# Performance work log

Measured on AMD Instinct MI355X. Metric: run time of the kernel, lower is better.

Reference implementation:

```python
import jax, jax.numpy as jnp
import numpy as np

B, T, H, NH, L, V, FF = 2, 1024, 1024, 16, 6, 8192, 4096
D = H // NH
EPS = 1e-5


def _ln(x, g, b):
    mu = jnp.mean(x, axis=-1, keepdims=True)
    var = jnp.mean(jnp.square(x - mu), axis=-1, keepdims=True)
    return (x - mu) * jax.lax.rsqrt(var + EPS) * g + b


def setup_inputs() -> dict:
    key = jax.random.key(0)
    ks = jax.random.split(key, 12)
    s = 1.0 / np.sqrt(H)
    return {
        "x": jax.random.randint(ks[0], (B, T), 0, V),
        "tok_emb": jax.random.normal(ks[1], (V, H), jnp.float32) * s,
        "pos_emb": jax.random.normal(ks[2], (1, T, H), jnp.float32) * s,
        "Wq": jax.random.normal(ks[3], (L, H, H), jnp.float32) * s,
        "bq": jnp.zeros((L, H), jnp.float32),
        "Wk": jax.random.normal(ks[4], (L, H, H), jnp.float32) * s,
        "bk": jnp.zeros((L, H), jnp.float32),
        "Wv": jax.random.normal(ks[5], (L, H, H), jnp.float32) * s,
        "bv": jnp.zeros((L, H), jnp.float32),
        "Wo": jax.random.normal(ks[6], (L, H, H), jnp.float32) * s,
        "bo": jnp.zeros((L, H), jnp.float32),
        "W1": jax.random.normal(ks[7], (L, H, FF), jnp.float32) * s,
        "b1": jnp.zeros((L, FF), jnp.float32),
        "W2": jax.random.normal(ks[8], (L, FF, H), jnp.float32) * (1.0 / np.sqrt(FF)),
        "b2": jnp.zeros((L, H), jnp.float32),
        "ln1_g": jnp.ones((L, H), jnp.float32),
        "ln1_b": jnp.zeros((L, H), jnp.float32),
        "ln2_g": jnp.ones((L, H), jnp.float32),
        "ln2_b": jnp.zeros((L, H), jnp.float32),
        "lnf_g": jnp.ones((H,), jnp.float32),
        "lnf_b": jnp.zeros((H,), jnp.float32),
        "headW": jax.random.normal(ks[9], (H, V), jnp.float32) * s,
        "headb": jnp.zeros((V,), jnp.float32),
    }


def _transformer(x, tok_emb, pos_emb, Wq, bq, Wk, bk, Wv, bv, Wo, bo,
                 W1, b1, W2, b2, ln1_g, ln1_b, ln2_g, ln2_b, lnf_g, lnf_b,
                 headW, headb):
    Tcur = x.shape[1]
    h = tok_emb[x] + pos_emb[:, :Tcur, :]            # [B,T,H]
    mask = jnp.tril(jnp.ones((Tcur, Tcur), bool))    # causal [T,T]
    scale = 1.0 / np.sqrt(D)

    def block(h, p):
        (wq, q_b, wk, k_b, wv, v_b, wo, o_b,
         w1, b1_, w2, b2_, g1, be1, g2, be2) = p
        q = (h @ wq + q_b).reshape(B, Tcur, NH, D)
        k = (h @ wk + k_b).reshape(B, Tcur, NH, D)
        v = (h @ wv + v_b).reshape(B, Tcur, NH, D)
        att = jnp.einsum('bqnd,bknd->bnqk', q, k) * scale
        att = jnp.where(mask, att, -jnp.inf)
        w = jax.nn.softmax(att, axis=-1)
        o = jnp.einsum('bnqk,bknd->bqnd', w, v).reshape(B, Tcur, H)
        h = _ln(h + (o @ wo + o_b), g1, be1)          # post-LN after attention
        m = jax.nn.gelu(h @ w1 + b1_, approximate=False) @ w2 + b2_
        h = _ln(h + m, g2, be2)                       # post-LN after MLP
        return h, None

    params = (Wq, bq, Wk, bk, Wv, bv, Wo, bo, W1, b1, W2, b2,
              ln1_g, ln1_b, ln2_g, ln2_b)
    h, _ = jax.lax.scan(block, h, params)
    h = _ln(h, lnf_g, lnf_b)
    return h @ headW + headb                          # [B,T,V]


def reference(x, tok_emb, pos_emb, Wq, bq, Wk, bk, Wv, bv, Wo, bo,
              W1, b1, W2, b2, ln1_g, ln1_b, ln2_g, ln2_b, lnf_g, lnf_b,
              headW, headb):
    return _transformer(x, tok_emb, pos_emb, Wq, bq, Wk, bk, Wv, bv, Wo, bo,
                        W1, b1, W2, b2, ln1_g, ln1_b, ln2_g, ln2_b,
                        lnf_g, lnf_b, headW, headb)
```

## Files before the change

### kernel.cpp

```cpp
#include <hip/hip_runtime.h>
#include <hip/hip_bf16.h>

#define DEV __device__ __forceinline__

typedef unsigned short u16;
typedef __attribute__((ext_vector_type(8))) short bf16x8;
typedef __attribute__((ext_vector_type(4))) float f32x4;

static constexpr int MB_ = 2;
static constexpr int T_  = 1024;
static constexpr int H_  = 1024;
static constexpr int NH_ = 16;
static constexpr int L_  = 6;
static constexpr int V_  = 8192;
static constexpr int FF_ = 4096;
static constexpr int M_  = MB_ * T_;
static constexpr int QKVN = 3 * H_;

DEV u16 f2bf(float x) {
  __hip_bfloat16 h = __float2bfloat16(x);
  return *reinterpret_cast<u16*>(&h);
}

__global__ __launch_bounds__(256) void embed_concat_kernel(
    const int* __restrict__ x, const float* __restrict__ tok,
    const float* __restrict__ pos, float* __restrict__ h, u16* __restrict__ hb,
    const float* __restrict__ bq, const float* __restrict__ bk,
    const float* __restrict__ bv, float* __restrict__ outb)
{
  int i = blockIdx.x;
  if (i < M_) {
    int t = threadIdx.x;
    int id = x[i];
    int tt = i & (T_ - 1);
    float4 a = *(const float4*)(tok + (size_t)id * H_ + t * 4);
    float4 b = *(const float4*)(pos + (size_t)tt * H_ + t * 4);
    float4 r = make_float4(a.x + b.x, a.y + b.y, a.z + b.z, a.w + b.w);
    *(float4*)(h + (size_t)i * H_ + t * 4) = r;
    ushort4 u = make_ushort4(f2bf(r.x), f2bf(r.y), f2bf(r.z), f2bf(r.w));
    *(ushort4*)(hb + (size_t)i * H_ + t * 4) = u;
  } else {
    int l = i - M_;
    for (int j = threadIdx.x; j < H_; j += 256) {
      outb[(size_t)l * QKVN + j]          = bq[(size_t)l * H_ + j];
      outb[(size_t)l * QKVN + H_ + j]     = bk[(size_t)l * H_ + j];
      outb[(size_t)l * QKVN + 2 * H_ + j] = bv[(size_t)l * H_ + j];
    }
  }
}

DEV void transpose_tile128s(float (*Ts)[65], const float* __restrict__ W,
                            u16* __restrict__ WT, int R, int C, int bx, int by)
{
  const int t = threadIdx.x;
  const int lr = t >> 4;
  const int lcq = (t & 15) * 4;
  #pragma unroll
  for (int si = 0; si < 2; ++si) {
    #pragma unroll
    for (int sj = 0; sj < 2; ++sj) {
      const int r0 = by * 128 + si * 64, c0 = bx * 128 + sj * 64;
      #pragma unroll
      for (int it = 0; it < 4; ++it) {
        int r = it * 16 + lr;
        float4 v = *(const float4*)(W + (size_t)(r0 + r) * C + c0 + lcq);
        Ts[r][lcq + 0] = v.x; Ts[r][lcq + 1] = v.y;
        Ts[r][lcq + 2] = v.z; Ts[r][lcq + 3] = v.w;
      }
      __syncthreads();
      #pragma unroll
      for (int it = 0; it < 4; ++it) {
        int n = it * 16 + lr;
        ushort4 u = make_ushort4(f2bf(Ts[lcq + 0][n]), f2bf(Ts[lcq + 1][n]),
                                 f2bf(Ts[lcq + 2][n]), f2bf(Ts[lcq + 3][n]));
        *(ushort4*)(WT + (size_t)(c0 + n) * R + r0 + lcq) = u;
      }
      __syncthreads();
    }
  }
}

DEV void transpose_layer_body(float (*Ts)[65], int t,
    const float* Wq, const float* Wk, const float* Wv, const float* Wo,
    const float* W1, const float* W2,
    u16* qkvT, u16* oT, u16* w1T, u16* w2T)
{
  if (t < 256) {
    int m = t >> 6, idx = t & 63, bx = idx & 7, by = idx >> 3;
    const float* W = (m == 0) ? Wq : (m == 1) ? Wk : (m == 2) ? Wv : Wo;
    u16* WT = (m == 3) ? oT : qkvT + (size_t)m * H_ * H_;
    transpose_tile128s(Ts, W, WT, H_, H_, bx, by);
  } else if (t < 512) {
    int idx = t - 256;
    transpose_tile128s(Ts, W1, w1T, H_, FF_, idx & 31, idx >> 5);
  } else {
    int idx = t - 512;
    transpose_tile128s(Ts, W2, w2T, FF_, H_, idx & 7, idx >> 3);
  }
}

__global__ __launch_bounds__(256) void transpose_layer_k(
    const float* __restrict__ Wq, const float* __restrict__ Wk,
    const float* __restrict__ Wv, const float* __restrict__ Wo,
    const float* __restrict__ W1, const float* __restrict__ W2,
    u16* qkvT, u16* oT, u16* w1T, u16* w2T)
{
  __shared__ float Ts[64][65];
  transpose_layer_body(Ts, blockIdx.x, Wq, Wk, Wv, Wo, W1, W2, qkvT, oT, w1T, w2T);
}


#define GLOAD_LDS16(g, l)                                              \
  __builtin_amdgcn_global_load_lds(                                    \
      (const __attribute__((address_space(1))) void*)(g),              \
      (__attribute__((address_space(3))) void*)(l), 16, 0, 0)

DEV void stage_t(const u16* __restrict__ G, int ldk, int r0g, int kofs,
                 u16* lds, int w, int lane)
{
  const int rl = ((lane >> 3) << 1) | ((lane >> 2) & 1);
  #pragma unroll
  for (int j = 0; j < 2; ++j) {
    const int row0 = w * 32 + j * 16;
    const int row = row0 + rl;
    const int c = (lane & 3) ^ (((row0 >> 1) + (lane >> 3)) & 3);
    const u16* g = G + (size_t)(r0g + row) * ldk + kofs + c * 8;
    GLOAD_LDS16(g, lds + row0 * 32);
  }
}

DEV bf16x8 frag3(const u16* lds, int rr, int ch) {
  return *(const bf16x8*)(lds + (rr >> 1) * 64 + (rr & 1) * 32 +
                          ((ch ^ ((rr >> 1) & 3)) * 8));
}

template<int N>
DEV void wait_vm_barrier() {
  asm volatile("s_waitcnt vmcnt(%0)" :: "n"(N) : "memory");
  __builtin_amdgcn_s_barrier();
}

DEV void comp3(const u16* As, const u16* Bs, f32x4 (&acc)[4][4],
               int wr, int wc, int lc, int lg)
{
  bf16x8 af[4], bv[4];
  #pragma unroll
  for (int mi = 0; mi < 4; ++mi)
    af[mi] = frag3(As, wr * 64 + mi * 16 + lc, lg);
  #pragma unroll
  for (int ni = 0; ni < 4; ++ni)
    bv[ni] = frag3(Bs, wc * 64 + ni * 16 + lc, lg);
  #pragma unroll
  for (int mi = 0; mi < 4; ++mi)
    #pragma unroll
    for (int ni = 0; ni < 4; ++ni)
      acc[mi][ni] = __builtin_amdgcn_mfma_f32_16x16x32_bf16(af[mi], bv[ni], acc[mi][ni], 0, 0, 0);
}

template<bool PARTIAL, bool DO_GELU, bool WF, bool WB>
DEV void gemm_body(u16* SMEM,
    const u16* __restrict__ A, const u16* __restrict__ BT,
    const float* __restrict__ bias, float* __restrict__ Cf,
    u16* __restrict__ Cb, float* __restrict__ P,
    int N, int K, int Ksub, int lid, int nwgx, int nwgy, int zid)
{
  const int tid = threadIdx.x;
  const int lane = tid & 63, w = tid >> 6;
  const int wr = w >> 1, wc = w & 1;
  const int lc = lane & 15, lg = lane >> 4;

  const int nwg = nwgx * nwgy;
  const int q8 = nwg >> 3, r8s = nwg & 7;
  const int xcd = lid & 7, ord = lid >> 3;
  const int sid = (xcd < r8s ? xcd * (q8 + 1) : r8s * (q8 + 1) + (xcd - r8s) * q8) + ord;
  const int m0 = (sid % nwgy) * 128, n0 = (sid / nwgy) * 128;

  const int kb = zid * Ksub;
  const int NT = Ksub >> 5;

  f32x4 acc[4][4];
  #pragma unroll
  for (int i = 0; i < 4; ++i)
    #pragma unroll
    for (int j = 0; j < 4; ++j) {
      f32x4 z = {0.f, 0.f, 0.f, 0.f};
      acc[i][j] = z;
    }

  auto STG = [&](int t, int b) {
    stage_t(A,  K, m0, kb + t * 32, SMEM + b * 4096, w, lane);
    stage_t(BT, K, n0, kb + t * 32, SMEM + 16384 + b * 4096, w, lane);
  };

  STG(0, 0);
  STG(1, 1);
  int t = 0;
  for (; t < NT - 2; ++t) {
    STG(t + 2, (t + 2) & 3);
    wait_vm_barrier<8>();
    comp3(SMEM + (t & 3) * 4096, SMEM + 16384 + (t & 3) * 4096, acc, wr, wc, lc, lg);
  }
  wait_vm_barrier<4>();
  comp3(SMEM + (t & 3) * 4096, SMEM + 16384 + (t & 3) * 4096, acc, wr, wc, lc, lg);
  ++t;
  wait_vm_barrier<0>();
  comp3(SMEM + (t & 3) * 4096, SMEM + 16384 + (t & 3) * 4096, acc, wr, wc, lc, lg);

  const size_t zofs = (size_t)zid * M_ * N;
  #pragma unroll
  for (int mi = 0; mi < 4; ++mi) {
    #pragma unroll
    for (int ni = 0; ni < 4; ++ni) {
      int gn = n0 + wc * 64 + ni * 16 + lc;
      float bvv = PARTIAL ? 0.f : bias[gn];
      #pragma unroll
      for (int r = 0; r < 4; ++r) {
        int gm = m0 + wr * 64 + mi * 16 + lg * 4 + r;
        float v = acc[mi][ni][r];
        if (PARTIAL) {
          P[zofs + (size_t)gm * N + gn] = v;
        } else {
          v += bvv;
          if (DO_GELU) v = 0.5f * v * (1.f + erff(v * 0.70710678118654752f));
          if (WF) Cf[(size_t)gm * N + gn] = v;
          if (WB) Cb[(size_t)gm * N + gn] = f2bf(v);
        }
      }
    }
  }
}

template<bool PARTIAL, bool DO_GELU, bool WF, bool WB>
__global__ __launch_bounds__(256, 2) void gemm3(
    const u16* __restrict__ A, const u16* __restrict__ BT,
    const float* __restrict__ bias, float* __restrict__ Cf,
    u16* __restrict__ Cb, float* __restrict__ P, int N, int K, int Ksub)
{
  __shared__ __align__(16) u16 SMEM[32768];
  gemm_body<PARTIAL, DO_GELU, WF, WB>(SMEM, A, BT, bias, Cf, Cb, P, N, K, Ksub,
      blockIdx.y * gridDim.x + blockIdx.x, gridDim.x, gridDim.y, blockIdx.z);
}

__global__ __launch_bounds__(256, 2) void gemmW1_fused(
    const u16* __restrict__ A, const u16* __restrict__ w1T,
    const float* __restrict__ bias, u16* __restrict__ m1,
    const float* nWq, const float* nWk, const float* nWv, const float* nWo,
    const float* nW1, const float* nW2,
    u16* nqkvT, u16* noT, u16* nw1T, u16* nw2T,
    const float* hW, u16* hT)
{
  __shared__ __align__(16) u16 SMEM[32768];
  const int id = blockIdx.x;
  if (id < 512) {
    gemm_body<false, true, false, true>(SMEM, A, w1T, bias, nullptr, m1, nullptr,
                                        FF_, H_, H_, id, 32, 16, 0);
  } else if (nWq) {
    float (*Ts)[65] = (float(*)[65])SMEM;
    transpose_layer_body(Ts, id - 512, nWq, nWk, nWv, nWo, nW1, nW2,
                         nqkvT, noT, nw1T, nw2T);
  } else {
    float (*Ts)[65] = (float(*)[65])SMEM;
    int idx = id - 512;
    transpose_tile128s(Ts, hW, hT, H_, V_, idx & 63, idx >> 6);
  }
}

__global__ __launch_bounds__(256) void ln_kernel(
    const float* __restrict__ X,
    const float* __restrict__ g, const float* __restrict__ be,
    u16* __restrict__ Hb)
{
  __shared__ float red[8];
  int row = blockIdx.x, t = threadIdx.x;
  int lane = t & 63, w = t >> 6;
  float4 v = *(const float4*)(X + (size_t)row * H_ + t * 4);
  float s = v.x + v.y + v.z + v.w;
  float q = v.x * v.x + v.y * v.y + v.z * v.z + v.w * v.w;
  #pragma unroll
  for (int o = 1; o < 64; o <<= 1) { s += __shfl_xor(s, o); q += __shfl_xor(q, o); }
  if (lane == 0) { red[w] = s; red[4 + w] = q; }
  __syncthreads();
  float S = red[0] + red[1] + red[2] + red[3];
  float Q = red[4] + red[5] + red[6] + red[7];
  float mu  = S * (1.f / H_);
  float var = Q * (1.f / H_) - mu * mu;
  float inv = rsqrtf(var + 1e-5f);
  float4 gv = *(const float4*)(g  + t * 4);
  float4 bv = *(const float4*)(be + t * 4);
  ushort4 u = make_ushort4(f2bf((v.x - mu) * inv * gv.x + bv.x),
                           f2bf((v.y - mu) * inv * gv.y + bv.y),
                           f2bf((v.z - mu) * inv * gv.z + bv.z),
                           f2bf((v.w - mu) * inv * gv.w + bv.w));
  *(ushort4*)(Hb + (size_t)row * H_ + t * 4) = u;
}

__global__ __launch_bounds__(256) void ln2_kernel(
    const float* __restrict__ P, int S,
    const float* __restrict__ bias,
    const float* __restrict__ g, const float* __restrict__ be,
    float* __restrict__ h, u16* __restrict__ hb)
{
  __shared__ float red[8];
  int row = blockIdx.x, t = threadIdx.x;
  int lane = t & 63, w = t >> 6;
  float4 v = *(const float4*)(h + (size_t)row * H_ + t * 4);
  float4 bb = *(const float4*)(bias + t * 4);
  v.x += bb.x; v.y += bb.y; v.z += bb.z; v.w += bb.w;
  for (int s0 = 0; s0 < S; ++s0) {
    float4 p = *(const float4*)(P + (size_t)s0 * M_ * H_ + (size_t)row * H_ + t * 4);
    v.x += p.x; v.y += p.y; v.z += p.z; v.w += p.w;
  }
  float s = v.x + v.y + v.z + v.w;
  float q = v.x * v.x + v.y * v.y + v.z * v.z + v.w * v.w;
  #pragma unroll
  for (int o = 1; o < 64; o <<= 1) { s += __shfl_xor(s, o); q += __shfl_xor(q, o); }
  if (lane == 0) { red[w] = s; red[4 + w] = q; }
  __syncthreads();
  float S1 = red[0] + red[1] + red[2] + red[3];
  float Q1 = red[4] + red[5] + red[6] + red[7];
  float mu  = S1 * (1.f / H_);
  float var = Q1 * (1.f / H_) - mu * mu;
  float inv = rsqrtf(var + 1e-5f);
  float4 gv = *(const float4*)(g  + t * 4);
  float4 bv = *(const float4*)(be + t * 4);
  float o0 = (v.x - mu) * inv * gv.x + bv.x;
  float o1 = (v.y - mu) * inv * gv.y + bv.y;
  float o2 = (v.z - mu) * inv * gv.z + bv.z;
  float o3 = (v.w - mu) * inv * gv.w + bv.w;
  *(float4*)(h + (size_t)row * H_ + t * 4) = make_float4(o0, o1, o2, o3);
  ushort4 u = make_ushort4(f2bf(o0), f2bf(o1), f2bf(o2), f2bf(o3));
  *(ushort4*)(hb + (size_t)row * H_ + t * 4) = u;
}

__global__ __launch_bounds__(256) void attn_kernel(
    const u16* __restrict__ qkv, u16* __restrict__ Og)
{
  __shared__ __align__(16) u16 Ks[2][64][72];
  __shared__ __align__(16) u16 Vs[2][64][72];
  __shared__ __align__(16) u16 QPs[4][16][72];

  const int qb = gridDim.x - 1 - blockIdx.x;
  const int bh = blockIdx.y;
  const int b = bh >> 4, hh = bh & 15;
  const int q0 = qb * 64;
  const size_t base  = ((size_t)b * T_) * QKVN + (size_t)hh * 64;
  const size_t baseO = ((size_t)b * T_) * H_ + (size_t)hh * 64;

  const int tid = threadIdx.x;
  const int lane = tid & 63, w = tid >> 6;
  const int lc = lane & 15, lg = lane >> 4;

  const int r8 = tid >> 3, d8 = (tid & 7) << 3;
  const int vk = tid & 31, vd = (tid >> 5) << 3;

  u16* Qflat = &QPs[0][0][0];

  bf16x8 kr[2], vr[2];
  #pragma unroll
  for (int i = 0; i < 2; ++i) {
    kr[i] = *(const bf16x8*)(qkv + base + H_ + (size_t)(i * 32 + r8) * QKVN + d8);
    vr[i] = *(const bf16x8*)(qkv + base + 2 * H_ + (size_t)(i * 32 + vk) * QKVN + vd);
  }
  #pragma unroll
  for (int i = 0; i < 2; ++i)
    *(bf16x8*)(Qflat + (size_t)(i * 32 + r8) * 72 + d8) =
      *(const bf16x8*)(qkv + base + (size_t)(q0 + i * 32 + r8) * QKVN + d8);
  #pragma unroll
  for (int i = 0; i < 2; ++i) {
    *(bf16x8*)&Ks[0][i * 32 + r8][d8] = kr[i];
    #pragma unroll
    for (int j = 0; j < 8; ++j) Vs[0][vd + j][i * 32 + vk] = ((const u16*)&vr[i])[j];
  }
  __syncthreads();
  bf16x8 aq0 = *(const bf16x8*)(Qflat + (size_t)(w * 16 + lc) * 72 + lg * 8);
  bf16x8 aq1 = *(const bf16x8*)(Qflat + (size_t)(w * 16 + lc) * 72 + 32 + lg * 8);

  float m_r[4], l_r[4];
  f32x4 oa[4];
  #pragma unroll
  for (int i = 0; i < 4; ++i) {
    m_r[i] = -1e30f; l_r[i] = 0.f;
    f32x4 z = {0.f, 0.f, 0.f, 0.f};
    oa[i] = z;
  }
  const float sc2 = 0.125f * 1.4426950408889634f;

  for (int kv = 0; kv <= qb; ++kv) {
    const int cur = kv & 1, nxt = cur ^ 1;
    if (kv < qb) {
      #pragma unroll
      for (int i = 0; i < 2; ++i) {
        kr[i] = *(const bf16x8*)(qkv + base + H_ + (size_t)((kv + 1) * 64 + i * 32 + r8) * QKVN + d8);
        vr[i] = *(const bf16x8*)(qkv + base + 2 * H_ + (size_t)((kv + 1) * 64 + i * 32 + vk) * QKVN + vd);
      }
    }

    f32x4 sfr[4];
    #pragma unroll
    for (int ni = 0; ni < 4; ++ni) { f32x4 z = {0.f,0.f,0.f,0.f}; sfr[ni] = z; }
    #pragma unroll
    for (int ni = 0; ni < 4; ++ni) {
      bf16x8 bk0 = *(const bf16x8*)&Ks[cur][ni * 16 + lc][lg * 8];
      bf16x8 bk1 = *(const bf16x8*)&Ks[cur][ni * 16 + lc][32 + lg * 8];
      sfr[ni] = __builtin_amdgcn_mfma_f32_16x16x32_bf16(aq0, bk0, sfr[ni], 0, 0, 0);
      sfr[ni] = __builtin_amdgcn_mfma_f32_16x16x32_bf16(aq1, bk1, sfr[ni], 0, 0, 0);
    }
    if (kv == qb) {
      #pragma unroll
      for (int ni = 0; ni < 4; ++ni)
        #pragma unroll
        for (int r = 0; r < 4; ++r)
          if (ni * 16 + lc > w * 16 + lg * 4 + r) sfr[ni][r] = -1e30f;
    }
    #pragma unroll
    for (int r = 0; r < 4; ++r) {
      float pm = fmaxf(fmaxf(sfr[0][r], sfr[1][r]), fmaxf(sfr[2][r], sfr[3][r]));
      pm = fmaxf(pm, __shfl_xor(pm, 1));
      pm = fmaxf(pm, __shfl_xor(pm, 2));
      pm = fmaxf(pm, __shfl_xor(pm, 4));
      pm = fmaxf(pm, __shfl_xor(pm, 8));
      float mn = fmaxf(m_r[r], pm);
      float al = exp2f(sc2 * (m_r[r] - mn));
      m_r[r] = mn; l_r[r] *= al;
      #pragma unroll
      for (int f = 0; f < 4; ++f) oa[f][r] *= al;
      float rs = 0.f;
      #pragma unroll
      for (int ni = 0; ni < 4; ++ni) {
        float p = exp2f(sc2 * (sfr[ni][r] - mn));
        sfr[ni][r] = p; rs += p;
      }
      rs += __shfl_xor(rs, 1); rs += __shfl_xor(rs, 2);
      rs += __shfl_xor(rs, 4); rs += __shfl_xor(rs, 8);
      l_r[r] += rs;
    }
    #pragma unroll
    for (int ni = 0; ni < 4; ++ni)
      #pragma unroll
      for (int r = 0; r < 4; ++r)
        QPs[w][lg * 4 + r][ni * 16 + lc] = f2bf(sfr[ni][r]);
    bf16x8 ap0 = *(const bf16x8*)&QPs[w][lc][lg * 8];
    bf16x8 ap1 = *(const bf16x8*)&QPs[w][lc][32 + lg * 8];
    #pragma unroll
    for (int f = 0; f < 4; ++f) {
      bf16x8 bv0 = *(const bf16x8*)&Vs[cur][f * 16 + lc][lg * 8];
      bf16x8 bv1 = *(const bf16x8*)&Vs[cur][f * 16 + lc][32 + lg * 8];
      oa[f] = __builtin_amdgcn_mfma_f32_16x16x32_bf16(ap0, bv0, oa[f], 0, 0, 0);
      oa[f] = __builtin_amdgcn_mfma_f32_16x16x32_bf16(ap1, bv1, oa[f], 0, 0, 0);
    }

    if (kv < qb) {
      #pragma unroll
      for (int i = 0; i < 2; ++i) {
        *(bf16x8*)&Ks[nxt][i * 32 + r8][d8] = kr[i];
        #pragma unroll
        for (int j = 0; j < 8; ++j) Vs[nxt][vd + j][i * 32 + vk] = ((const u16*)&vr[i])[j];
      }
      __syncthreads();
    }
  }

  #pragma unroll
  for (int r = 0; r < 4; ++r) {
    float inv = 1.f / l_r[r];
    int grow = q0 + w * 16 + lg * 4 + r;
    #pragma unroll
    for (int f = 0; f < 4; ++f)
      Og[baseO + (size_t)grow * H_ + f * 16 + lc] = f2bf(oa[f][r] * inv);
  }
}

extern "C" void kernel_launch(void* const* d_in, const int* in_sizes, int n_in,
                              void* d_out, int out_size, void* d_ws, size_t ws_size,
                              hipStream_t stream)
{
  const int*   x    = (const int*)  d_in[0];
  const float* tok  = (const float*)d_in[1];
  const float* pos  = (const float*)d_in[2];
  const float* Wq   = (const float*)d_in[3];
  const float* bq   = (const float*)d_in[4];
  const float* Wk   = (const float*)d_in[5];
  const float* bk   = (const float*)d_in[6];
  const float* Wv   = (const float*)d_in[7];
  const float* bv   = (const float*)d_in[8];
  const float* Wo   = (const float*)d_in[9];
  const float* bo   = (const float*)d_in[10];
  const float* W1   = (const float*)d_in[11];
  const float* b1   = (const float*)d_in[12];
  const float* W2   = (const float*)d_in[13];
  const float* b2   = (const float*)d_in[14];
  const float* g1   = (const float*)d_in[15];
  const float* be1  = (const float*)d_in[16];
  const float* g2   = (const float*)d_in[17];
  const float* be2  = (const float*)d_in[18];
  const float* gf   = (const float*)d_in[19];
  const float* bef  = (const float*)d_in[20];
  const float* hW   = (const float*)d_in[21];
  const float* hbias= (const float*)d_in[22];
  float* out = (float*)d_out;

  char* wsp = (char*)d_ws;
  size_t off = 0;
  auto alloc = [&](size_t bytes) -> void* {
    void* p = wsp + off;
    off += (bytes + 255) & ~(size_t)255;
    return p;
  };
  float* h    = (float*)alloc((size_t)M_ * H_ * 4);
  u16*   hb   = (u16*)  alloc((size_t)M_ * H_ * 2);
  u16*   qkv  = (u16*)  alloc((size_t)M_ * QKVN * 2);
  u16*   ob_  = (u16*)  alloc((size_t)M_ * H_ * 2);
  u16*   m1   = (u16*)  alloc((size_t)M_ * FF_ * 2);
  float* P    = (float*)alloc((size_t)4 * M_ * H_ * 4);
  u16*   hT   = (u16*)  alloc((size_t)V_ * H_ * 2);
  u16*   qkvT = (u16*)  alloc((size_t)QKVN * H_ * 2);
  u16*   oT   = (u16*)  alloc((size_t)H_ * H_ * 2);
  u16*   w1Tb = (u16*)  alloc((size_t)2 * H_ * FF_ * 2);
  u16*   w2Tb = (u16*)  alloc((size_t)2 * FF_ * H_ * 2);
  float* bqkv = (float*)alloc((size_t)L_ * QKVN * 4);
  (void)in_sizes; (void)n_in; (void)out_size; (void)ws_size;

  auto w1T = [&](int l) { return w1Tb + (size_t)(l & 1) * H_ * FF_; };
  auto w2T = [&](int l) { return w2Tb + (size_t)(l & 1) * FF_ * H_; };

  embed_concat_kernel<<<M_ + L_, 256, 0, stream>>>(x, tok, pos, h, hb,
                                                   bq, bk, bv, bqkv);
  transpose_layer_k<<<768, 256, 0, stream>>>(
      Wq, Wk, Wv, Wo, W1, W2, qkvT, oT, w1T(0), w2T(0));

  for (int l = 0; l < L_; ++l) {
    gemm3<false, false, false, true><<<dim3(QKVN / 128, M_ / 128, 1), 256, 0, stream>>>(
        hb, qkvT, bqkv + (size_t)l * QKVN, nullptr, qkv, nullptr, QKVN, H_, H_);
    attn_kernel<<<dim3(T_ / 64, MB_ * NH_), 256, 0, stream>>>(qkv, ob_);
    gemm3<true, false, false, false><<<dim3(H_ / 128, M_ / 128, 4), 256, 0, stream>>>(
        ob_, oT, nullptr, nullptr, nullptr, P, H_, H_, H_ / 4);
    ln2_kernel<<<M_, 256, 0, stream>>>(P, 4, bo + l * H_, g1 + l * H_, be1 + l * H_, h, hb);
    if (l + 1 < L_) {
      int nl = l + 1;
      gemmW1_fused<<<512 + 768, 256, 0, stream>>>(
          hb, w1T(l), b1 + (size_t)l * FF_, m1,
          Wq + (size_t)nl * H_ * H_, Wk + (size_t)nl * H_ * H_,
          Wv + (size_t)nl * H_ * H_, Wo + (size_t)nl * H_ * H_,
          W1 + (size_t)nl * H_ * FF_, W2 + (size_t)nl * FF_ * H_,
          qkvT, oT, w1T(nl), w2T(nl), nullptr, nullptr);
    } else {
      gemmW1_fused<<<512 + 512, 256, 0, stream>>>(
          hb, w1T(l), b1 + (size_t)l * FF_, m1,
          nullptr, nullptr, nullptr, nullptr, nullptr, nullptr,
          nullptr, nullptr, nullptr, nullptr, hW, hT);
    }
    gemm3<true, false, false, false><<<dim3(H_ / 128, M_ / 128, 4), 256, 0, stream>>>(
        m1, w2T(l), nullptr, nullptr, nullptr, P, H_, FF_, FF_ / 4);
    ln2_kernel<<<M_, 256, 0, stream>>>(P, 4, b2 + l * H_, g2 + l * H_, be2 + l * H_, h, hb);
  }

  ln_kernel<<<M_, 256, 0, stream>>>(h, gf, bef, hb);
  gemm3<false, false, true, false><<<dim3(V_ / 128, M_ / 128, 1), 256, 0, stream>>>(
      hb, hT, hbias, out, nullptr, nullptr, V_, H_, H_);
}
```

Before: 1.061 ms.

## Store split-K partials in bf16, fuse final LN, prioritize attention MFMA

Split-K GEMM partial sums are now written and read as bf16 instead of fp32, halving the partial-buffer traffic between the O-proj/W2 GEMMs and the LN kernels. The final layer norm is folded into the last ln2_kernel launch, which drops one kernel and one pass over h. The attention MFMA sections are wrapped in s_setprio to favour the matrix waves. Rounding partials to bf16 before summation adds precision error.

```diff
diff --git a/kernel.cpp b/kernel.cpp
--- a/kernel.cpp
+++ b/kernel.cpp
@@ -20,6 +20,12 @@
 DEV u16 f2bf(float x) {
   __hip_bfloat16 h = __float2bfloat16(x);
   return *reinterpret_cast<u16*>(&h);
+}
+DEV float bf2f(u16 v) {
+  unsigned u = (unsigned)v << 16;
+  float f;
+  __builtin_memcpy(&f, &u, 4);
+  return f;
 }
 
 __global__ __launch_bounds__(256) void embed_concat_kernel(
@@ -161,7 +167,7 @@
 DEV void gemm_body(u16* SMEM,
     const u16* __restrict__ A, const u16* __restrict__ BT,
     const float* __restrict__ bias, float* __restrict__ Cf,
-    u16* __restrict__ Cb, float* __restrict__ P,
+    u16* __restrict__ Cb, u16* __restrict__ Pb,
     int N, int K, int Ksub, int lid, int nwgx, int nwgy, int zid)
 {
   const int tid = threadIdx.x;
@@ -218,7 +224,7 @@
         int gm = m0 + wr * 64 + mi * 16 + lg * 4 + r;
         float v = acc[mi][ni][r];
         if (PARTIAL) {
-          P[zofs + (size_t)gm * N + gn] = v;
+          Pb[zofs + (size_t)gm * N + gn] = f2bf(v);
         } else {
           v += bvv;
           if (DO_GELU) v = 0.5f * v * (1.f + erff(v * 0.70710678118654752f));
@@ -234,10 +240,10 @@
 __global__ __launch_bounds__(256, 2) void gemm3(
     const u16* __restrict__ A, const u16* __restrict__ BT,
     const float* __restrict__ bias, float* __restrict__ Cf,
-    u16* __restrict__ Cb, float* __restrict__ P, int N, int K, int Ksub)
+    u16* __restrict__ Cb, u16* __restrict__ Pb, int N, int K, int Ksub)
 {
   __shared__ __align__(16) u16 SMEM[32768];
-  gemm_body<PARTIAL, DO_GELU, WF, WB>(SMEM, A, BT, bias, Cf, Cb, P, N, K, Ksub,
+  gemm_body<PARTIAL, DO_GELU, WF, WB>(SMEM, A, BT, bias, Cf, Cb, Pb, N, K, Ksub,
       blockIdx.y * gridDim.x + blockIdx.x, gridDim.x, gridDim.y, blockIdx.z);
 }
 
@@ -265,39 +271,11 @@
   }
 }
 
-__global__ __launch_bounds__(256) void ln_kernel(
-    const float* __restrict__ X,
-    const float* __restrict__ g, const float* __restrict__ be,
-    u16* __restrict__ Hb)
-{
-  __shared__ float red[8];
-  int row = blockIdx.x, t = threadIdx.x;
-  int lane = t & 63, w = t >> 6;
-  float4 v = *(const float4*)(X + (size_t)row * H_ + t * 4);
-  float s = v.x + v.y + v.z + v.w;
-  float q = v.x * v.x + v.y * v.y + v.z * v.z + v.w * v.w;
-  #pragma unroll
-  for (int o = 1; o < 64; o <<= 1) { s += __shfl_xor(s, o); q += __shfl_xor(q, o); }
-  if (lane == 0) { red[w] = s; red[4 + w] = q; }
-  __syncthreads();
-  float S = red[0] + red[1] + red[2] + red[3];
-  float Q = red[4] + red[5] + red[6] + red[7];
-  float mu  = S * (1.f / H_);
-  float var = Q * (1.f / H_) - mu * mu;
-  float inv = rsqrtf(var + 1e-5f);
-  float4 gv = *(const float4*)(g  + t * 4);
-  float4 bv = *(const float4*)(be + t * 4);
-  ushort4 u = make_ushort4(f2bf((v.x - mu) * inv * gv.x + bv.x),
-                           f2bf((v.y - mu) * inv * gv.y + bv.y),
-                           f2bf((v.z - mu) * inv * gv.z + bv.z),
-                           f2bf((v.w - mu) * inv * gv.w + bv.w));
-  *(ushort4*)(Hb + (size_t)row * H_ + t * 4) = u;
-}
-
 __global__ __launch_bounds__(256) void ln2_kernel(
-    const float* __restrict__ P, int S,
+    const u16* __restrict__ Pb, int S,
     const float* __restrict__ bias,
     const float* __restrict__ g, const float* __restrict__ be,
+    const float* __restrict__ gf, const float* __restrict__ bef,
     float* __restrict__ h, u16* __restrict__ hb)
 {
   __shared__ float red[8];
@@ -307,8 +285,8 @@
   float4 bb = *(const float4*)(bias + t * 4);
   v.x += bb.x; v.y += bb.y; v.z += bb.z; v.w += bb.w;
   for (int s0 = 0; s0 < S; ++s0) {
-    float4 p = *(const float4*)(P + (size_t)s0 * M_ * H_ + (size_t)row * H_ + t * 4);
-    v.x += p.x; v.y += p.y; v.z += p.z; v.w += p.w;
+    ushort4 p = *(const ushort4*)(Pb + (size_t)s0 * M_ * H_ + (size_t)row * H_ + t * 4);
+    v.x += bf2f(p.x); v.y += bf2f(p.y); v.z += bf2f(p.z); v.w += bf2f(p.w);
   }
   float s = v.x + v.y + v.z + v.w;
   float q = v.x * v.x + v.y * v.y + v.z * v.z + v.w * v.w;
@@ -327,9 +305,31 @@
   float o1 = (v.y - mu) * inv * gv.y + bv.y;
   float o2 = (v.z - mu) * inv * gv.z + bv.z;
   float o3 = (v.w - mu) * inv * gv.w + bv.w;
-  *(float4*)(h + (size_t)row * H_ + t * 4) = make_float4(o0, o1, o2, o3);
-  ushort4 u = make_ushort4(f2bf(o0), f2bf(o1), f2bf(o2), f2bf(o3));
-  *(ushort4*)(hb + (size_t)row * H_ + t * 4) = u;
+  if (gf == nullptr) {
+    *(float4*)(h + (size_t)row * H_ + t * 4) = make_float4(o0, o1, o2, o3);
+    ushort4 u = make_ushort4(f2bf(o0), f2bf(o1), f2bf(o2), f2bf(o3));
+    *(ushort4*)(hb + (size_t)row * H_ + t * 4) = u;
+  } else {
+    float s2 = o0 + o1 + o2 + o3;
+    float q2 = o0 * o0 + o1 * o1 + o2 * o2 + o3 * o3;
+    #pragma unroll
+    for (int o = 1; o < 64; o <<= 1) { s2 += __shfl_xor(s2, o); q2 += __shfl_xor(q2, o); }
+    __syncthreads();
+    if (lane == 0) { red[w] = s2; red[4 + w] = q2; }
+    __syncthreads();
+    float S2 = red[0] + red[1] + red[2] + red[3];
+    float Q2 = red[4] + red[5] + red[6] + red[7];
+    float mu2  = S2 * (1.f / H_);
+    float var2 = Q2 * (1.f / H_) - mu2 * mu2;
+    float inv2 = rsqrtf(var2 + 1e-5f);
+    float4 gv2 = *(const float4*)(gf  + t * 4);
+    float4 bv2 = *(const float4*)(bef + t * 4);
+    ushort4 u = make_ushort4(f2bf((o0 - mu2) * inv2 * gv2.x + bv2.x),
+                             f2bf((o1 - mu2) * inv2 * gv2.y + bv2.y),
+                             f2bf((o2 - mu2) * inv2 * gv2.z + bv2.z),
+                             f2bf((o3 - mu2) * inv2 * gv2.w + bv2.w));
+    *(ushort4*)(hb + (size_t)row * H_ + t * 4) = u;
+  }
 }
 
 __global__ __launch_bounds__(256) void attn_kernel(
@@ -398,6 +398,7 @@
     f32x4 sfr[4];
     #pragma unroll
     for (int ni = 0; ni < 4; ++ni) { f32x4 z = {0.f,0.f,0.f,0.f}; sfr[ni] = z; }
+    __builtin_amdgcn_s_setprio(1);
     #pragma unroll
     for (int ni = 0; ni < 4; ++ni) {
       bf16x8 bk0 = *(const bf16x8*)&Ks[cur][ni * 16 + lc][lg * 8];
@@ -405,6 +406,7 @@
       sfr[ni] = __builtin_amdgcn_mfma_f32_16x16x32_bf16(aq0, bk0, sfr[ni], 0, 0, 0);
       sfr[ni] = __builtin_amdgcn_mfma_f32_16x16x32_bf16(aq1, bk1, sfr[ni], 0, 0, 0);
     }
+    __builtin_amdgcn_s_setprio(0);
     if (kv == qb) {
       #pragma unroll
       for (int ni = 0; ni < 4; ++ni)
@@ -441,6 +443,7 @@
         QPs[w][lg * 4 + r][ni * 16 + lc] = f2bf(sfr[ni][r]);
     bf16x8 ap0 = *(const bf16x8*)&QPs[w][lc][lg * 8];
     bf16x8 ap1 = *(const bf16x8*)&QPs[w][lc][32 + lg * 8];
+    __builtin_amdgcn_s_setprio(1);
     #pragma unroll
     for (int f = 0; f < 4; ++f) {
       bf16x8 bv0 = *(const bf16x8*)&Vs[cur][f * 16 + lc][lg * 8];
@@ -448,6 +451,7 @@
       oa[f] = __builtin_amdgcn_mfma_f32_16x16x32_bf16(ap0, bv0, oa[f], 0, 0, 0);
       oa[f] = __builtin_amdgcn_mfma_f32_16x16x32_bf16(ap1, bv1, oa[f], 0, 0, 0);
     }
+    __builtin_amdgcn_s_setprio(0);
 
     if (kv < qb) {
       #pragma unroll
@@ -511,7 +515,7 @@
   u16*   qkv  = (u16*)  alloc((size_t)M_ * QKVN * 2);
   u16*   ob_  = (u16*)  alloc((size_t)M_ * H_ * 2);
   u16*   m1   = (u16*)  alloc((size_t)M_ * FF_ * 2);
-  float* P    = (float*)alloc((size_t)4 * M_ * H_ * 4);
+  u16*   Pb   = (u16*)  alloc((size_t)4 * M_ * H_ * 2);
   u16*   hT   = (u16*)  alloc((size_t)V_ * H_ * 2);
   u16*   qkvT = (u16*)  alloc((size_t)QKVN * H_ * 2);
   u16*   oT   = (u16*)  alloc((size_t)H_ * H_ * 2);
@@ -533,8 +537,9 @@
         hb, qkvT, bqkv + (size_t)l * QKVN, nullptr, qkv, nullptr, QKVN, H_, H_);
     attn_kernel<<<dim3(T_ / 64, MB_ * NH_), 256, 0, stream>>>(qkv, ob_);
     gemm3<true, false, false, false><<<dim3(H_ / 128, M_ / 128, 4), 256, 0, stream>>>(
-        ob_, oT, nullptr, nullptr, nullptr, P, H_, H_, H_ / 4);
-    ln2_kernel<<<M_, 256, 0, stream>>>(P, 4, bo + l * H_, g1 + l * H_, be1 + l * H_, h, hb);
+        ob_, oT, nullptr, nullptr, nullptr, Pb, H_, H_, H_ / 4);
+    ln2_kernel<<<M_, 256, 0, stream>>>(Pb, 4, bo + l * H_, g1 + l * H_, be1 + l * H_,
+                                       nullptr, nullptr, h, hb);
     if (l + 1 < L_) {
       int nl = l + 1;
       gemmW1_fused<<<512 + 768, 256, 0, stream>>>(
@@ -550,11 +555,16 @@
           nullptr, nullptr, nullptr, nullptr, hW, hT);
     }
     gemm3<true, false, false, false><<<dim3(H_ / 128, M_ / 128, 4), 256, 0, stream>>>(
-        m1, w2T(l), nullptr, nullptr, nullptr, P, H_, FF_, FF_ / 4);
-    ln2_kernel<<<M_, 256, 0, stream>>>(P, 4, b2 + l * H_, g2 + l * H_, be2 + l * H_, h, hb);
-  }
-
-  ln_kernel<<<M_, 256, 0, stream>>>(h, gf, bef, hb);
+        m1, w2T(l), nullptr, nullptr, nullptr, Pb, H_, FF_, FF_ / 4);
+    if (l + 1 < L_) {
+      ln2_kernel<<<M_, 256, 0, stream>>>(Pb, 4, b2 + l * H_, g2 + l * H_, be2 + l * H_,
+                                         nullptr, nullptr, h, hb);
+    } else {
+      ln2_kernel<<<M_, 256, 0, stream>>>(Pb, 4, b2 + l * H_, g2 + l * H_, be2 + l * H_,
+                                         gf, bef, h, hb);
+    }
+  }
+
   gemm3<false, false, true, false><<<dim3(V_ / 128, M_ / 128, 1), 256, 0, stream>>>(
       hb, hT, hbias, out, nullptr, nullptr, V_, H_, H_);
 }
```

Result: faster. 1.006 ms (-5.2%).
